# Performance work log

Measured on AMD Instinct MI355X. Metric: run time of the kernel, lower is better.

## Reference

```python
import jax, jax.numpy as jnp
import numpy as np

GAMMA = 1.0

def setup_inputs() -> dict:
    key = jax.random.key(0)
    kx, ky = jax.random.split(key)
    x = jax.random.normal(kx, (8192, 64), dtype=jnp.float32)
    y = jax.random.normal(ky, (8192, 64), dtype=jnp.float32)
    return {"x": x, "y": y}

def reference(x, y):
    # RBF Gram matrix: exp(-gamma * ||x_i - y_j||^2)
    # materializing the [N, M, D] broadcast difference.
    x_sq = jnp.sum(x * x, axis=-1)            # [N]
    y_sq = jnp.sum(y * y, axis=-1)            # [M]
    cross = jnp.einsum('nd,md->nm', x, y)     # [N, M]
    sq_norm = x_sq[:, None] + y_sq[None, :] - 2.0 * cross
    sq_norm = jnp.maximum(sq_norm, 0.0)       # guard tiny negatives from cancellation
    return jnp.exp(-GAMMA * sq_norm)
```

## Files before the change

### kernel.cpp

```cpp
#include <hip/hip_runtime.h>
#include <hip/hip_bf16.h>

typedef __attribute__((ext_vector_type(8))) short short8;
typedef __attribute__((ext_vector_type(4))) float f32x4;

#define NROWS 8192
#define DDIM  64

#if defined(__has_builtin) && __has_builtin(__builtin_amdgcn_exp2f)
#define FAST_EXP2(x) __builtin_amdgcn_exp2f(x)
#else
#define FAST_EXP2(x) exp2f(x)
#endif

#define LOG2E 1.4426950408889634f

__device__ __forceinline__ unsigned short f32_to_bf16_bits(float f) {
    unsigned u = __float_as_uint(f);
    unsigned r = u + 0x7FFFu + ((u >> 16) & 1u);
    return (unsigned short)(r >> 16);
}
__device__ __forceinline__ float bf16_bits_to_f32(unsigned short b) {
    return __uint_as_float(((unsigned)b) << 16);
}

__global__ __launch_bounds__(256) void prep_kernel(
    const float* __restrict__ x, const float* __restrict__ y,
    short* __restrict__ xh, short* __restrict__ xl,
    short* __restrict__ yh, short* __restrict__ yl,
    float* __restrict__ xsl, float* __restrict__ ysl)
{
    int gwid = (int)((blockIdx.x * blockDim.x + threadIdx.x) >> 6);
    int lane = threadIdx.x & 63;

    const float* src; short* dh; short* dl; float* dsq; int row;
    if (gwid < NROWS) { src = x; dh = xh; dl = xl; dsq = xsl; row = gwid; }
    else              { src = y; dh = yh; dl = yl; dsq = ysl; row = gwid - NROWS; }

    float v = src[row * DDIM + lane];
    unsigned short hb = f32_to_bf16_bits(v);
    float hf = bf16_bits_to_f32(hb);
    unsigned short lb = f32_to_bf16_bits(v - hf);

    dh[row * DDIM + lane] = (short)hb;
    dl[row * DDIM + lane] = (short)lb;

    float sq = v * v;
    #pragma unroll
    for (int off = 32; off; off >>= 1) sq += __shfl_xor(sq, off);
    if (lane == 0) dsq[row] = sq * LOG2E;
}

__global__ __launch_bounds__(256) void rbf_mfma_kernel(
    const short* __restrict__ xh, const short* __restrict__ xl,
    const short* __restrict__ yh, const short* __restrict__ yl,
    const float* __restrict__ xsl, const float* __restrict__ ysl,
    float* __restrict__ out)
{
    int bid = blockIdx.x;
    int bi = bid >> 6;
    int bj = bid & 63;
    int tid = threadIdx.x;
    int wid = tid >> 6, lane = tid & 63;
    int wr = wid >> 1, wc = wid & 1;
    int g = lane >> 4, l15 = lane & 15;

    int arow = bi * 128 + wr * 64 + l15;
    int brow = bj * 128 + wc * 64 + l15;

    f32x4 acc[4][4];
    #pragma unroll
    for (int i = 0; i < 4; ++i)
        #pragma unroll
        for (int j = 0; j < 4; ++j)
            acc[i][j] = (f32x4){0.f, 0.f, 0.f, 0.f};

    #pragma unroll
    for (int ks = 0; ks < 2; ++ks) {
        int koff = ks * 32 + g * 8;
        short8 ah[4], al[4], bh[4], bl[4];
        #pragma unroll
        for (int f = 0; f < 4; ++f) {
            long aoff = (long)(arow + f * 16) * DDIM + koff;
            long boff = (long)(brow + f * 16) * DDIM + koff;
            ah[f] = *(const short8*)(xh + aoff);
            al[f] = *(const short8*)(xl + aoff);
            bh[f] = *(const short8*)(yh + boff);
            bl[f] = *(const short8*)(yl + boff);
        }
        #pragma unroll
        for (int mf = 0; mf < 4; ++mf)
            #pragma unroll
            for (int nf = 0; nf < 4; ++nf) {
                acc[mf][nf] = __builtin_amdgcn_mfma_f32_16x16x32_bf16(ah[mf], bh[nf], acc[mf][nf], 0, 0, 0);
                acc[mf][nf] = __builtin_amdgcn_mfma_f32_16x16x32_bf16(ah[mf], bl[nf], acc[mf][nf], 0, 0, 0);
                acc[mf][nf] = __builtin_amdgcn_mfma_f32_16x16x32_bf16(al[mf], bh[nf], acc[mf][nf], 0, 0, 0);
            }
    }

    float ysl_r[4];
    #pragma unroll
    for (int nf = 0; nf < 4; ++nf)
        ysl_r[nf] = ysl[bj * 128 + wc * 64 + nf * 16 + l15];

    #pragma unroll
    for (int mf = 0; mf < 4; ++mf) {
        #pragma unroll
        for (int r = 0; r < 4; ++r) {
            int m = bi * 128 + wr * 64 + mf * 16 + g * 4 + r;
            float xs = xsl[m];
            float* orow = out + (long)m * NROWS + (bj * 128 + wc * 64 + l15);
            #pragma unroll
            for (int nf = 0; nf < 4; ++nf) {
                float t = __builtin_fmaf(2.0f * LOG2E, acc[mf][nf][r], -(xs + ysl_r[nf]));
                t = fminf(t, 0.0f);
                __builtin_nontemporal_store(FAST_EXP2(t), orow + nf * 16);
            }
        }
    }
}

__global__ __launch_bounds__(256) void rbf_fused_kernel(
    const float* __restrict__ x, const float* __restrict__ y,
    float* __restrict__ out)
{
    int bid = blockIdx.x;
    int bi = bid >> 6, bj = bid & 63;
    int tid = threadIdx.x;
    int wid = tid >> 6, lane = tid & 63;
    int wr = wid >> 1, wc = wid & 1;
    int g = lane >> 4, l15 = lane & 15;

    int abase = bi * 128 + wr * 64;
    int bbase = bj * 128 + wc * 64;

    float xs_own = 0.f, ys_own = 0.f;
    {
        const float4* px = (const float4*)(x + (long)(abase + lane) * DDIM);
        const float4* py = (const float4*)(y + (long)(bbase + lane) * DDIM);
        #pragma unroll
        for (int i = 0; i < 16; ++i) {
            float4 v = px[i];
            xs_own += v.x * v.x + v.y * v.y + v.z * v.z + v.w * v.w;
            float4 w = py[i];
            ys_own += w.x * w.x + w.y * w.y + w.z * w.z + w.w * w.w;
        }
    }

    f32x4 acc[4][4];
    #pragma unroll
    for (int i = 0; i < 4; ++i)
        #pragma unroll
        for (int j = 0; j < 4; ++j)
            acc[i][j] = (f32x4){0.f, 0.f, 0.f, 0.f};

    #pragma unroll
    for (int ks = 0; ks < 2; ++ks) {
        int koff = ks * 32 + g * 8;
        short8 ah[4], al[4], bh[4], bl[4];
        #pragma unroll
        for (int f = 0; f < 4; ++f) {
            const float* pa = x + (long)(abase + f * 16 + l15) * DDIM + koff;
            const float* pb = y + (long)(bbase + f * 16 + l15) * DDIM + koff;
            #pragma unroll
            for (int i = 0; i < 8; ++i) {
                float va = pa[i];
                unsigned short hba = f32_to_bf16_bits(va);
                ah[f][i] = (short)hba;
                al[f][i] = (short)f32_to_bf16_bits(va - bf16_bits_to_f32(hba));
                float vb = pb[i];
                unsigned short hbb = f32_to_bf16_bits(vb);
                bh[f][i] = (short)hbb;
                bl[f][i] = (short)f32_to_bf16_bits(vb - bf16_bits_to_f32(hbb));
            }
        }
        #pragma unroll
        for (int mf = 0; mf < 4; ++mf)
            #pragma unroll
            for (int nf = 0; nf < 4; ++nf) {
                acc[mf][nf] = __builtin_amdgcn_mfma_f32_16x16x32_bf16(ah[mf], bh[nf], acc[mf][nf], 0, 0, 0);
                acc[mf][nf] = __builtin_amdgcn_mfma_f32_16x16x32_bf16(ah[mf], bl[nf], acc[mf][nf], 0, 0, 0);
                acc[mf][nf] = __builtin_amdgcn_mfma_f32_16x16x32_bf16(al[mf], bh[nf], acc[mf][nf], 0, 0, 0);
            }
    }

    #pragma unroll
    for (int mf = 0; mf < 4; ++mf) {
        #pragma unroll
        for (int r = 0; r < 4; ++r) {
            int m_rel = mf * 16 + g * 4 + r;
            float xs = __shfl(xs_own, m_rel);
            int m = abase + m_rel;
            #pragma unroll
            for (int nf = 0; nf < 4; ++nf) {
                int n_rel = nf * 16 + l15;
                float ys = __shfl(ys_own, n_rel);
                int n = bbase + n_rel;
                float s = fmaxf(xs + ys - 2.0f * acc[mf][nf][r], 0.0f);
                __builtin_nontemporal_store(__expf(-s), &out[(long)m * NROWS + n]);
            }
        }
    }
}

extern "C" void kernel_launch(void* const* d_in, const int* in_sizes, int n_in,
                              void* d_out, int out_size, void* d_ws, size_t ws_size,
                              hipStream_t stream) {
    const float* x = (const float*)d_in[0];
    const float* y = (const float*)d_in[1];
    float* out = (float*)d_out;

    const size_t plane = (size_t)NROWS * DDIM * sizeof(short);
    const size_t sqsz  = (size_t)NROWS * sizeof(float);
    const size_t need  = 4 * plane + 2 * sqsz;

    if (ws_size >= need && d_ws != nullptr) {
        char* ws = (char*)d_ws;
        short* xh = (short*)(ws);
        short* xl = (short*)(ws + plane);
        short* yh = (short*)(ws + 2 * plane);
        short* yl = (short*)(ws + 3 * plane);
        float* xsl = (float*)(ws + 4 * plane);
        float* ysl = (float*)(ws + 4 * plane + sqsz);

        prep_kernel<<<(2 * NROWS) / 4, 256, 0, stream>>>(x, y, xh, xl, yh, yl, xsl, ysl);
        rbf_mfma_kernel<<<64 * 64, 256, 0, stream>>>(xh, xl, yh, yl, xsl, ysl, out);
    } else {
        rbf_fused_kernel<<<64 * 64, 256, 0, stream>>>(x, y, out);
    }
}
```

Baseline: 300.6 us.

## Stage output tile through LDS for coalesced 16-byte stores and swizzle block order

The epilogue first writes the exp results into a padded shared-memory tile, one 64-row half at a time. It then stores them to global memory as contiguous float4 rows, replacing the scattered 4-byte per-lane stores. The block index is also permuted so that consecutive blocks spread across bi rows, which changes the cache and DRAM-channel access pattern. In exchange the kernel uses about 33 KB of LDS, adds two barriers per phase, and leaves half the waves idle during each write phase.

```diff
diff --git a/kernel.cpp b/kernel.cpp
--- a/kernel.cpp
+++ b/kernel.cpp
@@ -57,9 +57,12 @@
     const float* __restrict__ xsl, const float* __restrict__ ysl,
     float* __restrict__ out)
 {
+    __shared__ float lt[64][132];
+
     int bid = blockIdx.x;
-    int bi = bid >> 6;
-    int bj = bid & 63;
+    int swz = ((bid & 7) << 9) | (bid >> 3);
+    int bi = swz >> 6;
+    int bj = swz & 63;
     int tid = threadIdx.x;
     int wid = tid >> 6, lane = tid & 63;
     int wr = wid >> 1, wc = wid & 1;
@@ -103,20 +106,37 @@
     for (int nf = 0; nf < 4; ++nf)
         ysl_r[nf] = ysl[bj * 128 + wc * 64 + nf * 16 + l15];
 
-    #pragma unroll
-    for (int mf = 0; mf < 4; ++mf) {
-        #pragma unroll
-        for (int r = 0; r < 4; ++r) {
-            int m = bi * 128 + wr * 64 + mf * 16 + g * 4 + r;
-            float xs = xsl[m];
-            float* orow = out + (long)m * NROWS + (bj * 128 + wc * 64 + l15);
-            #pragma unroll
-            for (int nf = 0; nf < 4; ++nf) {
-                float t = __builtin_fmaf(2.0f * LOG2E, acc[mf][nf][r], -(xs + ysl_r[nf]));
-                t = fminf(t, 0.0f);
-                __builtin_nontemporal_store(FAST_EXP2(t), orow + nf * 16);
-            }
-        }
+    long obase = (long)(bi * 128) * NROWS + bj * 128;
+    int r32 = tid >> 5;
+    int c4  = (tid & 31) << 2;
+
+    #pragma unroll
+    for (int ph = 0; ph < 2; ++ph) {
+        if (wr == ph) {
+            #pragma unroll
+            for (int mf = 0; mf < 4; ++mf) {
+                #pragma unroll
+                for (int r = 0; r < 4; ++r) {
+                    int lrow = mf * 16 + g * 4 + r;
+                    float xs = xsl[bi * 128 + ph * 64 + lrow];
+                    #pragma unroll
+                    for (int nf = 0; nf < 4; ++nf) {
+                        float t = __builtin_fmaf(2.0f * LOG2E, acc[mf][nf][r],
+                                                 -(xs + ysl_r[nf]));
+                        lt[lrow][wc * 64 + nf * 16 + l15] = FAST_EXP2(fminf(t, 0.0f));
+                    }
+                }
+            }
+        }
+        __syncthreads();
+        #pragma unroll
+        for (int i = 0; i < 8; ++i) {
+            int lrow = r32 + i * 8;
+            f32x4 v = *(const f32x4*)&lt[lrow][c4];
+            __builtin_nontemporal_store(v,
+                (f32x4*)(out + obase + (long)(ph * 64 + lrow) * NROWS + c4));
+        }
+        __syncthreads();
     }
 }
 
```

Result: slower. 311.9 us (+3.7%).

## Shrink MFMA per-wave tile to 16x128 and raise occupancy

Applied to the files above, without the earlier changes.

Restructures the MFMA kernel so each wave computes a 16-row by 128-column strip with a single accumulator per 16x16 tile, streaming the epilogue per tile. The block tile becomes 64x128 and the grid doubles, with launch bounds requesting 6 blocks per CU. The aim is lower register pressure and more waves in flight to hide the store-bound epilogue. The cost is less operand reuse: B fragments are reloaded by every wave and by twice as many blocks.

```diff
diff --git a/kernel.cpp b/kernel.cpp
--- a/kernel.cpp
+++ b/kernel.cpp
@@ -51,7 +51,7 @@
     if (lane == 0) dsq[row] = sq * LOG2E;
 }
 
-__global__ __launch_bounds__(256) void rbf_mfma_kernel(
+__global__ __launch_bounds__(256, 6) void rbf_mfma_kernel(
     const short* __restrict__ xh, const short* __restrict__ xl,
     const short* __restrict__ yh, const short* __restrict__ yl,
     const float* __restrict__ xsl, const float* __restrict__ ysl,
@@ -62,60 +62,47 @@
     int bj = bid & 63;
     int tid = threadIdx.x;
     int wid = tid >> 6, lane = tid & 63;
-    int wr = wid >> 1, wc = wid & 1;
     int g = lane >> 4, l15 = lane & 15;
 
-    int arow = bi * 128 + wr * 64 + l15;
-    int brow = bj * 128 + wc * 64 + l15;
-
-    f32x4 acc[4][4];
-    #pragma unroll
-    for (int i = 0; i < 4; ++i)
-        #pragma unroll
-        for (int j = 0; j < 4; ++j)
-            acc[i][j] = (f32x4){0.f, 0.f, 0.f, 0.f};
-
+    int mbase = bi * 64 + wid * 16;
+    int arow  = mbase + l15;
+
+    short8 ah[2], al[2];
     #pragma unroll
     for (int ks = 0; ks < 2; ++ks) {
-        int koff = ks * 32 + g * 8;
-        short8 ah[4], al[4], bh[4], bl[4];
-        #pragma unroll
-        for (int f = 0; f < 4; ++f) {
-            long aoff = (long)(arow + f * 16) * DDIM + koff;
-            long boff = (long)(brow + f * 16) * DDIM + koff;
-            ah[f] = *(const short8*)(xh + aoff);
-            al[f] = *(const short8*)(xl + aoff);
-            bh[f] = *(const short8*)(yh + boff);
-            bl[f] = *(const short8*)(yl + boff);
-        }
-        #pragma unroll
-        for (int mf = 0; mf < 4; ++mf)
-            #pragma unroll
-            for (int nf = 0; nf < 4; ++nf) {
-                acc[mf][nf] = __builtin_amdgcn_mfma_f32_16x16x32_bf16(ah[mf], bh[nf], acc[mf][nf], 0, 0, 0);
-                acc[mf][nf] = __builtin_amdgcn_mfma_f32_16x16x32_bf16(ah[mf], bl[nf], acc[mf][nf], 0, 0, 0);
-                acc[mf][nf] = __builtin_amdgcn_mfma_f32_16x16x32_bf16(al[mf], bh[nf], acc[mf][nf], 0, 0, 0);
-            }
-    }
-
-    float ysl_r[4];
-    #pragma unroll
-    for (int nf = 0; nf < 4; ++nf)
-        ysl_r[nf] = ysl[bj * 128 + wc * 64 + nf * 16 + l15];
-
-    #pragma unroll
-    for (int mf = 0; mf < 4; ++mf) {
+        long aoff = (long)arow * DDIM + ks * 32 + g * 8;
+        ah[ks] = *(const short8*)(xh + aoff);
+        al[ks] = *(const short8*)(xl + aoff);
+    }
+
+    f32x4 xs4 = *(const f32x4*)(xsl + mbase + g * 4);
+    float ys_r[8];
+    #pragma unroll
+    for (int nf = 0; nf < 8; ++nf)
+        ys_r[nf] = ysl[bj * 128 + nf * 16 + l15];
+
+    #pragma unroll
+    for (int nf = 0; nf < 8; ++nf) {
+        int n0 = bj * 128 + nf * 16;
+        long b0 = (long)(n0 + l15) * DDIM + g * 8;
+        short8 bh0 = *(const short8*)(yh + b0);
+        short8 bl0 = *(const short8*)(yl + b0);
+        short8 bh1 = *(const short8*)(yh + b0 + 32);
+        short8 bl1 = *(const short8*)(yl + b0 + 32);
+
+        f32x4 acc = (f32x4){0.f, 0.f, 0.f, 0.f};
+        acc = __builtin_amdgcn_mfma_f32_16x16x32_bf16(ah[0], bh0, acc, 0, 0, 0);
+        acc = __builtin_amdgcn_mfma_f32_16x16x32_bf16(ah[0], bl0, acc, 0, 0, 0);
+        acc = __builtin_amdgcn_mfma_f32_16x16x32_bf16(al[0], bh0, acc, 0, 0, 0);
+        acc = __builtin_amdgcn_mfma_f32_16x16x32_bf16(ah[1], bh1, acc, 0, 0, 0);
+        acc = __builtin_amdgcn_mfma_f32_16x16x32_bf16(ah[1], bl1, acc, 0, 0, 0);
+        acc = __builtin_amdgcn_mfma_f32_16x16x32_bf16(al[1], bh1, acc, 0, 0, 0);
+
         #pragma unroll
         for (int r = 0; r < 4; ++r) {
-            int m = bi * 128 + wr * 64 + mf * 16 + g * 4 + r;
-            float xs = xsl[m];
-            float* orow = out + (long)m * NROWS + (bj * 128 + wc * 64 + l15);
-            #pragma unroll
-            for (int nf = 0; nf < 4; ++nf) {
-                float t = __builtin_fmaf(2.0f * LOG2E, acc[mf][nf][r], -(xs + ysl_r[nf]));
-                t = fminf(t, 0.0f);
-                __builtin_nontemporal_store(FAST_EXP2(t), orow + nf * 16);
-            }
+            float t = __builtin_fmaf(2.0f * LOG2E, acc[r], -(xs4[r] + ys_r[nf]));
+            __builtin_nontemporal_store(FAST_EXP2(fminf(t, 0.0f)),
+                out + (long)(mbase + g * 4 + r) * NROWS + n0 + l15);
         }
     }
 }
@@ -224,7 +211,7 @@
         float* ysl = (float*)(ws + 4 * plane + sqsz);
 
         prep_kernel<<<(2 * NROWS) / 4, 256, 0, stream>>>(x, y, xh, xl, yh, yl, xsl, ysl);
-        rbf_mfma_kernel<<<64 * 64, 256, 0, stream>>>(xh, xl, yh, yl, xsl, ysl, out);
+        rbf_mfma_kernel<<<128 * 64, 256, 0, stream>>>(xh, xl, yh, yl, xsl, ysl, out);
     } else {
         rbf_fused_kernel<<<64 * 64, 256, 0, stream>>>(x, y, out);
     }
```

New measurement: 362.9 us. +20.7%, slower.
